# Kernel tuning notes

Measured on AMD Instinct MI355X. Metric: run time of the kernel, lower is better.

The kernel has to match this reference:

```python
import jax, jax.numpy as jnp
import numpy as np

B, S, D, H = 2, 2048, 1024, 16
DK = D // H


def setup_inputs() -> dict:
    key = jax.random.key(0)
    ks = jax.random.split(key, 12)
    q = jax.random.normal(ks[0], (B, S, D), dtype=jnp.float32)
    k = jax.random.normal(ks[1], (B, S, D), dtype=jnp.float32)
    v = jax.random.normal(ks[2], (B, S, D), dtype=jnp.float32)
    # causal mask: positions where mask == 0 are masked out
    mask = jnp.tril(jnp.ones((S, S), dtype=jnp.int32))[None, None, :, :]
    s = 1.0 / np.sqrt(D)
    Wq = jax.random.uniform(ks[3], (D, D), jnp.float32, -s, s)
    bq = jax.random.uniform(ks[4], (D,), jnp.float32, -s, s)
    Wk = jax.random.uniform(ks[5], (D, D), jnp.float32, -s, s)
    bk = jax.random.uniform(ks[6], (D,), jnp.float32, -s, s)
    Wv = jax.random.uniform(ks[7], (D, D), jnp.float32, -s, s)
    bv = jax.random.uniform(ks[8], (D,), jnp.float32, -s, s)
    Wo = jax.random.uniform(ks[9], (D, D), jnp.float32, -s, s)
    bo = jax.random.uniform(ks[10], (D,), jnp.float32, -s, s)
    return {"q": q, "k": k, "v": v, "mask": mask,
            "Wq": Wq, "bq": bq, "Wk": Wk, "bk": bk,
            "Wv": Wv, "bv": bv, "Wo": Wo, "bo": bo}


def reference(q, k, v, mask, Wq, bq, Wk, bk, Wv, bv, Wo, bo):
    b = q.shape[0]
    # linear projections (nn.Linear: x @ W.T + b), split into heads -> [b,h,s,dk]
    qh = (q @ Wq.T + bq).reshape(b, -1, H, DK).transpose(0, 2, 1, 3)
    kh = (k @ Wk.T + bk).reshape(b, -1, H, DK).transpose(0, 2, 1, 3)
    vh = (v @ Wv.T + bv).reshape(b, -1, H, DK).transpose(0, 2, 1, 3)
    scores = jnp.einsum('bhqd,bhkd->bhqk', qh, kh) / jnp.sqrt(jnp.float32(DK))
    scores = jnp.where(mask == 0, jnp.float32(-1e9), scores)
    attn = jax.nn.softmax(scores, axis=-1)  # dropout p=0.0 -> identity
    out = jnp.einsum('bhqk,bhkd->bhqd', attn, vh)
    out = out.transpose(0, 2, 1, 3).reshape(b, -1, D)
    return out @ Wo.T + bo
```

## Files before the change

kernel.cpp:

```cpp
#include <hip/hip_runtime.h>


typedef _Float16 f16;
typedef __attribute__((ext_vector_type(4))) float   f32x4;
typedef __attribute__((ext_vector_type(8))) _Float16 f16x8;

#define DEVI __device__ __forceinline__

static constexpr int S  = 2048;
static constexpr int D  = 1024;
static constexpr int KK = 1024;
static constexpr int M  = 4096;

DEVI void gload_lds16(const void* g, void* l) {
  __builtin_amdgcn_global_load_lds((const __attribute__((address_space(1))) void*)g,
                                   (__attribute__((address_space(3))) void*)l, 16, 0, 0);
}

DEVI f32x4 mfma16(f16x8 a, f16x8 b, f32x4 c) {
  return __builtin_amdgcn_mfma_f32_16x16x32_f16(a, b, c, 0, 0, 0);
}

DEVI int xorv(int row) { return ((row ^ (row >> 3)) & 7) << 4; }

__global__ __launch_bounds__(256) void cvt_kernel(const float* __restrict__ s0,
                                                  const float* __restrict__ s1,
                                                  const float* __restrict__ s2,
                                                  const float* __restrict__ s3,
                                                  f16* __restrict__ dst, int nper) {
  const float* s = blockIdx.y == 0 ? s0 : blockIdx.y == 1 ? s1 : blockIdx.y == 2 ? s2 : s3;
  f16* d = dst + (size_t)blockIdx.y * nper;
  const int i = (blockIdx.x * 256 + threadIdx.x) * 8;
  f32x4 a = *(const f32x4*)(s + i);
  f32x4 b = *(const f32x4*)(s + i + 4);
  f16x8 r;
#pragma unroll
  for (int j = 0; j < 4; ++j) { r[j] = (f16)a[j]; r[4 + j] = (f16)b[j]; }
  *(f16x8*)(d + i) = r;
}

DEVI void gemm_mainloop(const f16* __restrict__ A, const f16* __restrict__ W,
                        int m0, int n0, f16* As, f16* Bs, f32x4 acc[4][4]) {
  const int tid  = threadIdx.x;
  const int wid  = tid >> 6;
  const int lane = tid & 63;
  const int wr = wid >> 1, wc = wid & 1;

  const f32x4 z4 = {0.f, 0.f, 0.f, 0.f};
#pragma unroll
  for (int mi = 0; mi < 4; ++mi)
#pragma unroll
    for (int ni = 0; ni < 4; ++ni) acc[mi][ni] = z4;

  const int r0 = tid >> 2, c0 = (tid & 3) * 8;
  const int r1 = 64 + r0;
  const f16* Ag0 = A + (size_t)(m0 + r0) * KK + c0;
  const f16* Ag1 = A + (size_t)(m0 + r1) * KK + c0;
  const f16* Bg0 = W + (size_t)(n0 + r0) * KK + c0;
  const f16* Bg1 = W + (size_t)(n0 + r1) * KK + c0;
  f16* As0 = As + wid * 512;
  f16* As1 = As + 2048 + wid * 512;
  f16* Bs0 = Bs + wid * 512;
  f16* Bs1 = Bs + 2048 + wid * 512;

  const int arow = wr * 64 + (lane & 15);
  const int brow = wc * 64 + (lane & 15);
  const int ko   = (lane >> 4) * 8;

  for (int k0 = 0; k0 < KK; k0 += 32) {
    gload_lds16(Ag0 + k0, As0);
    gload_lds16(Ag1 + k0, As1);
    gload_lds16(Bg0 + k0, Bs0);
    gload_lds16(Bg1 + k0, Bs1);
    __syncthreads();
    f16x8 af[4], bf[4];
#pragma unroll
    for (int mi = 0; mi < 4; ++mi) af[mi] = *(const f16x8*)&As[(arow + mi * 16) * 32 + ko];
#pragma unroll
    for (int ni = 0; ni < 4; ++ni) bf[ni] = *(const f16x8*)&Bs[(brow + ni * 16) * 32 + ko];
#pragma unroll
    for (int mi = 0; mi < 4; ++mi)
#pragma unroll
      for (int ni = 0; ni < 4; ++ni)
        acc[mi][ni] = mfma16(af[mi], bf[ni], acc[mi][ni]);
    __syncthreads();
  }
}

__global__ __launch_bounds__(256, 2) void gemm_qkv_kernel(const f16* __restrict__ X,
                                                          const f16* __restrict__ Wp,
                                                          const float* __restrict__ b0,
                                                          const float* __restrict__ b1,
                                                          const float* __restrict__ b2,
                                                          f16* __restrict__ Hd) {
  __shared__ f16 As[128 * 32];
  __shared__ f16 Bs[128 * 32];
  const int z = blockIdx.z;
  const f16* A = X + (size_t)z * (M * KK);
  const f16* W = Wp + (size_t)z * (D * KK);
  const float* bias = z == 0 ? b0 : z == 1 ? b1 : b2;
  f16* dst = Hd + (size_t)z * (size_t)4194304;
  const float scale = (z == 0) ? 0.125f : 1.0f;
  const int m0 = blockIdx.y * 128, n0 = blockIdx.x * 128;

  f32x4 acc[4][4];
  gemm_mainloop(A, W, m0, n0, As, Bs, acc);

  const int lane = threadIdx.x & 63, wid = threadIdx.x >> 6;
  const int wr = wid >> 1, wc = wid & 1;
#pragma unroll
  for (int ni = 0; ni < 4; ++ni) {
    const int col = n0 + wc * 64 + ni * 16 + (lane & 15);
    const float bv = bias[col];
    const int h = col >> 6, dk = col & 63;
#pragma unroll
    for (int mi = 0; mi < 4; ++mi) {
#pragma unroll
      for (int r = 0; r < 4; ++r) {
        const int row = m0 + wr * 64 + mi * 16 + (lane >> 4) * 4 + r;
        const int bb = row >> 11, ss = row & 2047;
        dst[(size_t)((bb * 16 + h) * 2048 + ss) * 64 + dk] = (f16)((acc[mi][ni][r] + bv) * scale);
      }
    }
  }
}

__global__ __launch_bounds__(256, 2) void gemm_out_kernel(const f16* __restrict__ A,
                                                          const f16* __restrict__ W,
                                                          const float* __restrict__ bias,
                                                          float* __restrict__ out) {
  __shared__ f16 As[128 * 32];
  __shared__ f16 Bs[128 * 32];
  const int m0 = blockIdx.y * 128, n0 = blockIdx.x * 128;
  f32x4 acc[4][4];
  gemm_mainloop(A, W, m0, n0, As, Bs, acc);
  const int lane = threadIdx.x & 63, wid = threadIdx.x >> 6;
  const int wr = wid >> 1, wc = wid & 1;
#pragma unroll
  for (int ni = 0; ni < 4; ++ni) {
    const int col = n0 + wc * 64 + ni * 16 + (lane & 15);
    const float bv = bias[col];
#pragma unroll
    for (int mi = 0; mi < 4; ++mi) {
#pragma unroll
      for (int r = 0; r < 4; ++r) {
        const int row = m0 + wr * 64 + mi * 16 + (lane >> 4) * 4 + r;
        out[(size_t)row * 1024 + col] = acc[mi][ni][r] + bv;
      }
    }
  }
}

__global__ __launch_bounds__(256, 2) void attn_kernel(const f16* __restrict__ Qh,
                                                      const f16* __restrict__ Kh,
                                                      const f16* __restrict__ Vh,
                                                      f16* __restrict__ Ao) {
  __shared__ f16 Ks[64 * 64];
  __shared__ f16 Vt[64 * 64];
  __shared__ f16 Ps[4][32 * 64];

  const int tid = threadIdx.x, wid = tid >> 6, lane = tid & 63;
  const int bh = blockIdx.y;
  const int q0 = blockIdx.x * 128;
  const int qw = q0 + wid * 32;
  const size_t base = (size_t)bh * (S * 64);

  f16x8 aq[2][2];
#pragma unroll
  for (int mi = 0; mi < 2; ++mi)
#pragma unroll
    for (int ks = 0; ks < 2; ++ks)
      aq[mi][ks] = *(const f16x8*)&Qh[base + (size_t)(qw + mi * 16 + (lane & 15)) * 64 +
                                      ks * 32 + (lane >> 4) * 8];

  const f32x4 z4 = {0.f, 0.f, 0.f, 0.f};
  f32x4 o[2][4];
  float mrow[2][4], lrow[2][4];
#pragma unroll
  for (int mi = 0; mi < 2; ++mi)
#pragma unroll
    for (int r = 0; r < 4; ++r) { mrow[mi][r] = -1e30f; lrow[mi][r] = 0.f; }
#pragma unroll
  for (int mi = 0; mi < 2; ++mi)
#pragma unroll
    for (int dj = 0; dj < 4; ++dj) o[mi][dj] = z4;

  const int ntiles = q0 / 64 + 2;
  for (int t = 0; t < ntiles; ++t) {
    const int kv0 = t * 64;
    __syncthreads();

#pragma unroll
    for (int i = 0; i < 2; ++i) {
      const int sl = i * 256 + tid;
      const int row = sl >> 3;
      const int cb = (sl & 7) * 16;
      const int col = (cb ^ xorv(row)) >> 1;
      gload_lds16(Kh + base + (size_t)(kv0 + row) * 64 + col,
                  (char*)Ks + i * 4096 + wid * 1024);
    }
#pragma unroll
    for (int r2 = 0; r2 < 2; ++r2) {
      const int kv = r2 * 32 + (tid >> 3);
      const int dk0 = (tid & 7) * 8;
      f16x8 vv = *(const f16x8*)&Vh[base + (size_t)(kv0 + kv) * 64 + dk0];
#pragma unroll
      for (int j = 0; j < 8; ++j) {
        const int dk = dk0 + j;
        *(f16*)((char*)Vt + dk * 128 + ((kv * 2) ^ xorv(dk))) = vv[j];
      }
    }
    __syncthreads();

    if (kv0 <= qw + 31) {
      f32x4 sc[2][4];
#pragma unroll
      for (int mi = 0; mi < 2; ++mi)
#pragma unroll
        for (int nj = 0; nj < 4; ++nj) sc[mi][nj] = z4;
#pragma unroll
      for (int nj = 0; nj < 4; ++nj) {
        const int krow = nj * 16 + (lane & 15);
#pragma unroll
        for (int ks = 0; ks < 2; ++ks) {
          f16x8 bk = *(const f16x8*)((char*)Ks + krow * 128 +
                                     ((ks * 64 + (lane >> 4) * 16) ^ xorv(krow)));
          sc[0][nj] = mfma16(aq[0][ks], bk, sc[0][nj]);
          sc[1][nj] = mfma16(aq[1][ks], bk, sc[1][nj]);
        }
      }
      if (kv0 + 63 > qw) {
#pragma unroll
        for (int mi = 0; mi < 2; ++mi)
#pragma unroll
          for (int nj = 0; nj < 4; ++nj)
#pragma unroll
            for (int r = 0; r < 4; ++r) {
              const int qq = qw + mi * 16 + (lane >> 4) * 4 + r;
              const int kv = kv0 + nj * 16 + (lane & 15);
              if (kv > qq) sc[mi][nj][r] = -1e30f;
            }
      }
      float mnew[2][4], scl[2][4], psum[2][4];
#pragma unroll
      for (int mi = 0; mi < 2; ++mi)
#pragma unroll
        for (int r = 0; r < 4; ++r) {
          float mx = fmaxf(fmaxf(sc[mi][0][r], sc[mi][1][r]), fmaxf(sc[mi][2][r], sc[mi][3][r]));
#pragma unroll
          for (int off = 1; off < 16; off <<= 1) mx = fmaxf(mx, __shfl_xor(mx, off));
          const float mn = fmaxf(mrow[mi][r], mx);
          mnew[mi][r] = mn;
          scl[mi][r]  = exp2f((mrow[mi][r] - mn) * 1.44269504f);
          psum[mi][r] = 0.f;
        }
#pragma unroll
      for (int mi = 0; mi < 2; ++mi)
#pragma unroll
        for (int nj = 0; nj < 4; ++nj) {
#pragma unroll
          for (int r = 0; r < 4; ++r) {
            const float p = exp2f((sc[mi][nj][r] - mnew[mi][r]) * 1.44269504f);
            psum[mi][r] += p;
            const int ql = mi * 16 + (lane >> 4) * 4 + r;
            const int kvl = nj * 16 + (lane & 15);
            *(f16*)((char*)Ps[wid] + ql * 128 + ((kvl * 2) ^ xorv(ql))) = (f16)p;
          }
        }
#pragma unroll
      for (int mi = 0; mi < 2; ++mi)
#pragma unroll
        for (int r = 0; r < 4; ++r) {
          float ps = psum[mi][r];
#pragma unroll
          for (int off = 1; off < 16; off <<= 1) ps += __shfl_xor(ps, off);
          lrow[mi][r] = lrow[mi][r] * scl[mi][r] + ps;
          mrow[mi][r] = mnew[mi][r];
        }
#pragma unroll
      for (int mi = 0; mi < 2; ++mi)
#pragma unroll
        for (int dj = 0; dj < 4; ++dj)
#pragma unroll
          for (int r = 0; r < 4; ++r) o[mi][dj][r] *= scl[mi][r];
#pragma unroll
      for (int ks = 0; ks < 2; ++ks) {
        f16x8 pa[2];
#pragma unroll
        for (int mi = 0; mi < 2; ++mi) {
          const int ql = mi * 16 + (lane & 15);
          pa[mi] = *(const f16x8*)((char*)Ps[wid] + ql * 128 +
                                   ((ks * 64 + (lane >> 4) * 16) ^ xorv(ql)));
        }
#pragma unroll
        for (int dj = 0; dj < 4; ++dj) {
          const int dr = dj * 16 + (lane & 15);
          f16x8 bv = *(const f16x8*)((char*)Vt + dr * 128 +
                                     ((ks * 64 + (lane >> 4) * 16) ^ xorv(dr)));
          o[0][dj] = mfma16(pa[0], bv, o[0][dj]);
          o[1][dj] = mfma16(pa[1], bv, o[1][dj]);
        }
      }
    }
  }

  const int bb = bh >> 4, hh = bh & 15;
#pragma unroll
  for (int mi = 0; mi < 2; ++mi)
#pragma unroll
    for (int r = 0; r < 4; ++r) {
      const float inv = 1.0f / lrow[mi][r];
      const int qq = qw + mi * 16 + (lane >> 4) * 4 + r;
#pragma unroll
      for (int dj = 0; dj < 4; ++dj) {
        const int dk = dj * 16 + (lane & 15);
        Ao[(size_t)(bb * 2048 + qq) * 1024 + hh * 64 + dk] = (f16)(o[mi][dj][r] * inv);
      }
    }
}

extern "C" void kernel_launch(void* const* d_in, const int* in_sizes, int n_in,
                              void* d_out, int out_size, void* d_ws, size_t ws_size,
                              hipStream_t stream) {
  const float* q  = (const float*)d_in[0];
  const float* k  = (const float*)d_in[1];
  const float* v  = (const float*)d_in[2];
  const float* Wq = (const float*)d_in[4];  const float* bq = (const float*)d_in[5];
  const float* Wk = (const float*)d_in[6];  const float* bk = (const float*)d_in[7];
  const float* Wv = (const float*)d_in[8];  const float* bv = (const float*)d_in[9];
  const float* Wo = (const float*)d_in[10]; const float* bo = (const float*)d_in[11];
  float* out = (float*)d_out;

  char* ws = (char*)d_ws;
  f16* xb = (f16*)(ws);
  f16* wb = (f16*)(ws + 25165824);
  f16* hb = (f16*)(ws + 33554432);
  f16* ao = (f16*)(ws + 58720256);

  cvt_kernel<<<dim3(2048, 3), 256, 0, stream>>>(q, k, v, nullptr, xb, 4194304);
  cvt_kernel<<<dim3(512, 4), 256, 0, stream>>>(Wq, Wk, Wv, Wo, wb, 1048576);
  gemm_qkv_kernel<<<dim3(8, 32, 3), 256, 0, stream>>>(xb, wb, bq, bk, bv, hb);
  attn_kernel<<<dim3(16, 32), 256, 0, stream>>>(hb, hb + 4194304, hb + 8388608, ao);
  gemm_out_kernel<<<dim3(8, 32), 256, 0, stream>>>(ao, wb + 3 * 1048576, bo, out);
}
```

Measured before the change: 318.2 us.

## Pre-transpose V, shrink attention blocks to 64 queries, reverse-order scheduling

Adds a separate kernel that writes V transposed to workspace, so the attention kernel can load V tiles directly into LDS with async global-to-LDS loads instead of doing scalar scattered transposing stores. The attention block shrinks to 128 threads covering 64 query rows, with more blocks launched and the heaviest causal blocks dispatched first. It drops the per-wave skip check and raises MFMA wave priority around the matmul sections. In exchange it pays for an extra kernel launch and an extra pass over V through global memory, and reuses the input-conversion buffer region for the transposed V.

```diff
diff --git a/kernel.cpp b/kernel.cpp
--- a/kernel.cpp
+++ b/kernel.cpp
@@ -151,17 +151,43 @@
   }
 }
 
-__global__ __launch_bounds__(256, 2) void attn_kernel(const f16* __restrict__ Qh,
+__global__ __launch_bounds__(256) void vtr_kernel(const f16* __restrict__ Vh,
+                                                  f16* __restrict__ VhT) {
+  __shared__ f16 T[64][72];
+  const int bh = blockIdx.y;
+  const int s0 = blockIdx.x * 64;
+  const size_t base = (size_t)bh * (S * 64);
+  const int tid = threadIdx.x;
+#pragma unroll
+  for (int i = 0; i < 2; ++i) {
+    const int c = i * 256 + tid;
+    const int sr = c >> 3, sc = (c & 7) * 8;
+    f16x8 v = *(const f16x8*)&Vh[base + (size_t)(s0 + sr) * 64 + sc];
+    *(f16x8*)&T[sr][sc] = v;
+  }
+  __syncthreads();
+#pragma unroll
+  for (int i = 0; i < 2; ++i) {
+    const int c = i * 256 + tid;
+    const int dk = c >> 3, so = (c & 7) * 8;
+    f16x8 r;
+#pragma unroll
+    for (int j = 0; j < 8; ++j) r[j] = T[so + j][dk];
+    *(f16x8*)&VhT[base + (size_t)dk * S + s0 + so] = r;
+  }
+}
+
+__global__ __launch_bounds__(128, 3) void attn_kernel(const f16* __restrict__ Qh,
                                                       const f16* __restrict__ Kh,
-                                                      const f16* __restrict__ Vh,
+                                                      const f16* __restrict__ VhT,
                                                       f16* __restrict__ Ao) {
   __shared__ f16 Ks[64 * 64];
   __shared__ f16 Vt[64 * 64];
-  __shared__ f16 Ps[4][32 * 64];
+  __shared__ f16 Ps[2][32 * 64];
 
   const int tid = threadIdx.x, wid = tid >> 6, lane = tid & 63;
   const int bh = blockIdx.y;
-  const int q0 = blockIdx.x * 128;
+  const int q0 = ((int)gridDim.x - 1 - (int)blockIdx.x) * 64;
   const int qw = q0 + wid * 32;
   const size_t base = (size_t)bh * (S * 64);
 
@@ -185,123 +211,116 @@
 #pragma unroll
     for (int dj = 0; dj < 4; ++dj) o[mi][dj] = z4;
 
-  const int ntiles = q0 / 64 + 2;
+  const int ntiles = q0 / 64 + 1;
   for (int t = 0; t < ntiles; ++t) {
     const int kv0 = t * 64;
     __syncthreads();
 
 #pragma unroll
-    for (int i = 0; i < 2; ++i) {
-      const int sl = i * 256 + tid;
+    for (int i = 0; i < 4; ++i) {
+      const int sl = i * 128 + tid;
       const int row = sl >> 3;
       const int cb = (sl & 7) * 16;
       const int col = (cb ^ xorv(row)) >> 1;
       gload_lds16(Kh + base + (size_t)(kv0 + row) * 64 + col,
-                  (char*)Ks + i * 4096 + wid * 1024);
-    }
-#pragma unroll
-    for (int r2 = 0; r2 < 2; ++r2) {
-      const int kv = r2 * 32 + (tid >> 3);
-      const int dk0 = (tid & 7) * 8;
-      f16x8 vv = *(const f16x8*)&Vh[base + (size_t)(kv0 + kv) * 64 + dk0];
-#pragma unroll
-      for (int j = 0; j < 8; ++j) {
-        const int dk = dk0 + j;
-        *(f16*)((char*)Vt + dk * 128 + ((kv * 2) ^ xorv(dk))) = vv[j];
-      }
+                  (char*)Ks + (i * 128 + wid * 64) * 16);
+      gload_lds16(VhT + base + (size_t)row * S + kv0 + col,
+                  (char*)Vt + (i * 128 + wid * 64) * 16);
     }
     __syncthreads();
 
-    if (kv0 <= qw + 31) {
-      f32x4 sc[2][4];
+    f32x4 sc[2][4];
+#pragma unroll
+    for (int mi = 0; mi < 2; ++mi)
+#pragma unroll
+      for (int nj = 0; nj < 4; ++nj) sc[mi][nj] = z4;
+    __builtin_amdgcn_s_setprio(1);
+#pragma unroll
+    for (int nj = 0; nj < 4; ++nj) {
+      const int krow = nj * 16 + (lane & 15);
+#pragma unroll
+      for (int ks = 0; ks < 2; ++ks) {
+        f16x8 bk = *(const f16x8*)((char*)Ks + krow * 128 +
+                                   ((ks * 64 + (lane >> 4) * 16) ^ xorv(krow)));
+        sc[0][nj] = mfma16(aq[0][ks], bk, sc[0][nj]);
+        sc[1][nj] = mfma16(aq[1][ks], bk, sc[1][nj]);
+      }
+    }
+    __builtin_amdgcn_s_setprio(0);
+    if (kv0 + 63 > qw) {
 #pragma unroll
       for (int mi = 0; mi < 2; ++mi)
 #pragma unroll
-        for (int nj = 0; nj < 4; ++nj) sc[mi][nj] = z4;
+        for (int nj = 0; nj < 4; ++nj)
+#pragma unroll
+          for (int r = 0; r < 4; ++r) {
+            const int qq = qw + mi * 16 + (lane >> 4) * 4 + r;
+            const int kv = kv0 + nj * 16 + (lane & 15);
+            if (kv > qq) sc[mi][nj][r] = -1e30f;
+          }
+    }
+    float mnew[2][4], scl[2][4], psum[2][4];
+#pragma unroll
+    for (int mi = 0; mi < 2; ++mi)
+#pragma unroll
+      for (int r = 0; r < 4; ++r) {
+        float mx = fmaxf(fmaxf(sc[mi][0][r], sc[mi][1][r]), fmaxf(sc[mi][2][r], sc[mi][3][r]));
+#pragma unroll
+        for (int off = 1; off < 16; off <<= 1) mx = fmaxf(mx, __shfl_xor(mx, off));
+        const float mn = fmaxf(mrow[mi][r], mx);
+        mnew[mi][r] = mn;
+        scl[mi][r]  = exp2f((mrow[mi][r] - mn) * 1.44269504f);
+        psum[mi][r] = 0.f;
+      }
+#pragma unroll
+    for (int mi = 0; mi < 2; ++mi)
 #pragma unroll
       for (int nj = 0; nj < 4; ++nj) {
-        const int krow = nj * 16 + (lane & 15);
-#pragma unroll
-        for (int ks = 0; ks < 2; ++ks) {
-          f16x8 bk = *(const f16x8*)((char*)Ks + krow * 128 +
-                                     ((ks * 64 + (lane >> 4) * 16) ^ xorv(krow)));
-          sc[0][nj] = mfma16(aq[0][ks], bk, sc[0][nj]);
-          sc[1][nj] = mfma16(aq[1][ks], bk, sc[1][nj]);
+#pragma unroll
+        for (int r = 0; r < 4; ++r) {
+          const float p = exp2f((sc[mi][nj][r] - mnew[mi][r]) * 1.44269504f);
+          psum[mi][r] += p;
+          const int ql = mi * 16 + (lane >> 4) * 4 + r;
+          const int kvl = nj * 16 + (lane & 15);
+          *(f16*)((char*)Ps[wid] + ql * 128 + ((kvl * 2) ^ xorv(ql))) = (f16)p;
         }
       }
-      if (kv0 + 63 > qw) {
-#pragma unroll
-        for (int mi = 0; mi < 2; ++mi)
-#pragma unroll
-          for (int nj = 0; nj < 4; ++nj)
-#pragma unroll
-            for (int r = 0; r < 4; ++r) {
-              const int qq = qw + mi * 16 + (lane >> 4) * 4 + r;
-              const int kv = kv0 + nj * 16 + (lane & 15);
-              if (kv > qq) sc[mi][nj][r] = -1e30f;
-            }
-      }
-      float mnew[2][4], scl[2][4], psum[2][4];
-#pragma unroll
-      for (int mi = 0; mi < 2; ++mi)
-#pragma unroll
-        for (int r = 0; r < 4; ++r) {
-          float mx = fmaxf(fmaxf(sc[mi][0][r], sc[mi][1][r]), fmaxf(sc[mi][2][r], sc[mi][3][r]));
-#pragma unroll
-          for (int off = 1; off < 16; off <<= 1) mx = fmaxf(mx, __shfl_xor(mx, off));
-          const float mn = fmaxf(mrow[mi][r], mx);
-          mnew[mi][r] = mn;
-          scl[mi][r]  = exp2f((mrow[mi][r] - mn) * 1.44269504f);
-          psum[mi][r] = 0.f;
-        }
-#pragma unroll
-      for (int mi = 0; mi < 2; ++mi)
-#pragma unroll
-        for (int nj = 0; nj < 4; ++nj) {
-#pragma unroll
-          for (int r = 0; r < 4; ++r) {
-            const float p = exp2f((sc[mi][nj][r] - mnew[mi][r]) * 1.44269504f);
-            psum[mi][r] += p;
-            const int ql = mi * 16 + (lane >> 4) * 4 + r;
-            const int kvl = nj * 16 + (lane & 15);
-            *(f16*)((char*)Ps[wid] + ql * 128 + ((kvl * 2) ^ xorv(ql))) = (f16)p;
-          }
-        }
-#pragma unroll
-      for (int mi = 0; mi < 2; ++mi)
-#pragma unroll
-        for (int r = 0; r < 4; ++r) {
-          float ps = psum[mi][r];
-#pragma unroll
-          for (int off = 1; off < 16; off <<= 1) ps += __shfl_xor(ps, off);
-          lrow[mi][r] = lrow[mi][r] * scl[mi][r] + ps;
-          mrow[mi][r] = mnew[mi][r];
-        }
-#pragma unroll
-      for (int mi = 0; mi < 2; ++mi)
-#pragma unroll
-        for (int dj = 0; dj < 4; ++dj)
-#pragma unroll
-          for (int r = 0; r < 4; ++r) o[mi][dj][r] *= scl[mi][r];
-#pragma unroll
-      for (int ks = 0; ks < 2; ++ks) {
-        f16x8 pa[2];
-#pragma unroll
-        for (int mi = 0; mi < 2; ++mi) {
-          const int ql = mi * 16 + (lane & 15);
-          pa[mi] = *(const f16x8*)((char*)Ps[wid] + ql * 128 +
-                                   ((ks * 64 + (lane >> 4) * 16) ^ xorv(ql)));
-        }
-#pragma unroll
-        for (int dj = 0; dj < 4; ++dj) {
-          const int dr = dj * 16 + (lane & 15);
-          f16x8 bv = *(const f16x8*)((char*)Vt + dr * 128 +
-                                     ((ks * 64 + (lane >> 4) * 16) ^ xorv(dr)));
-          o[0][dj] = mfma16(pa[0], bv, o[0][dj]);
-          o[1][dj] = mfma16(pa[1], bv, o[1][dj]);
-        }
-      }
-    }
+#pragma unroll
+    for (int mi = 0; mi < 2; ++mi)
+#pragma unroll
+      for (int r = 0; r < 4; ++r) {
+        float ps = psum[mi][r];
+#pragma unroll
+        for (int off = 1; off < 16; off <<= 1) ps += __shfl_xor(ps, off);
+        lrow[mi][r] = lrow[mi][r] * scl[mi][r] + ps;
+        mrow[mi][r] = mnew[mi][r];
+      }
+#pragma unroll
+    for (int mi = 0; mi < 2; ++mi)
+#pragma unroll
+      for (int dj = 0; dj < 4; ++dj)
+#pragma unroll
+        for (int r = 0; r < 4; ++r) o[mi][dj][r] *= scl[mi][r];
+    __builtin_amdgcn_s_setprio(1);
+#pragma unroll
+    for (int ks = 0; ks < 2; ++ks) {
+      f16x8 pa[2];
+#pragma unroll
+      for (int mi = 0; mi < 2; ++mi) {
+        const int ql = mi * 16 + (lane & 15);
+        pa[mi] = *(const f16x8*)((char*)Ps[wid] + ql * 128 +
+                                 ((ks * 64 + (lane >> 4) * 16) ^ xorv(ql)));
+      }
+#pragma unroll
+      for (int dj = 0; dj < 4; ++dj) {
+        const int dr = dj * 16 + (lane & 15);
+        f16x8 bv = *(const f16x8*)((char*)Vt + dr * 128 +
+                                   ((ks * 64 + (lane >> 4) * 16) ^ xorv(dr)));
+        o[0][dj] = mfma16(pa[0], bv, o[0][dj]);
+        o[1][dj] = mfma16(pa[1], bv, o[1][dj]);
+      }
+    }
+    __builtin_amdgcn_s_setprio(0);
   }
 
   const int bb = bh >> 4, hh = bh & 15;
@@ -336,10 +355,12 @@
   f16* wb = (f16*)(ws + 25165824);
   f16* hb = (f16*)(ws + 33554432);
   f16* ao = (f16*)(ws + 58720256);
+  f16* vt = (f16*)(ws);
 
   cvt_kernel<<<dim3(2048, 3), 256, 0, stream>>>(q, k, v, nullptr, xb, 4194304);
   cvt_kernel<<<dim3(512, 4), 256, 0, stream>>>(Wq, Wk, Wv, Wo, wb, 1048576);
   gemm_qkv_kernel<<<dim3(8, 32, 3), 256, 0, stream>>>(xb, wb, bq, bk, bv, hb);
-  attn_kernel<<<dim3(16, 32), 256, 0, stream>>>(hb, hb + 4194304, hb + 8388608, ao);
+  vtr_kernel<<<dim3(32, 32), 256, 0, stream>>>(hb + 8388608, vt);
+  attn_kernel<<<dim3(32, 32), 128, 0, stream>>>(hb, hb + 4194304, vt, ao);
   gemm_out_kernel<<<dim3(8, 32), 256, 0, stream>>>(ao, wb + 3 * 1048576, bo, out);
 }
```

After: 417.9 us. 31.3% more time.
